# Performance work log

Measured on AMD Instinct MI355X. Metric: run time of the kernel, lower is better.

## Reference

```python
import jax, jax.numpy as jnp
import numpy as np

N_NODES = 100_000
N_EDGES = 3_200_000
IN_FEAT = 512
HIDDEN = 16
N_CLASSES = 7


def setup_inputs() -> dict:
    key = jax.random.key(0)
    kx, ke, kw1, kw2 = jax.random.split(key, 4)
    x = jax.random.normal(kx, (N_NODES, IN_FEAT), dtype=jnp.float32)
    edge_index = jax.random.randint(ke, (2, N_EDGES), 0, N_NODES, dtype=jnp.int64)
    W1 = jax.random.normal(kw1, (IN_FEAT, HIDDEN), dtype=jnp.float32) * (1.0 / np.sqrt(IN_FEAT))
    b1 = jnp.zeros((HIDDEN,), dtype=jnp.float32)
    W2 = jax.random.normal(kw2, (HIDDEN, N_CLASSES), dtype=jnp.float32) * (1.0 / np.sqrt(HIDDEN))
    b2 = jnp.zeros((N_CLASSES,), dtype=jnp.float32)
    return {"x": x, "edge_index": edge_index, "W1": W1, "b1": b1, "W2": W2, "b2": b2}


def _gcn_conv(x, edge_index, W, b):
    """GCNConv: h = D^{-1/2} (A + I) D^{-1/2} (x W) + b  (symmetric normalization, self-loops)."""
    n = x.shape[0]
    h = x @ W  # transform first (small out dim), then aggregate
    loop = jnp.arange(n, dtype=edge_index.dtype)
    src = jnp.concatenate([edge_index[0], loop])  # message sources (incl. self-loops)
    dst = jnp.concatenate([edge_index[1], loop])  # message destinations
    deg = jax.ops.segment_sum(jnp.ones_like(dst, dtype=h.dtype), dst, num_segments=n)
    dinv = jnp.where(deg > 0, jax.lax.rsqrt(deg), 0.0).astype(h.dtype)
    norm = dinv[src] * dinv[dst]                 # [E+N]
    msg = h[src] * norm[:, None]                 # gather + scale
    out = jax.ops.segment_sum(msg, dst, num_segments=n)  # scatter-add
    return out + b


def reference(x, edge_index, W1, b1, W2, b2):
    h = jax.nn.relu(_gcn_conv(x, edge_index, W1, b1))
    # dropout is identity in eval mode
    logits = _gcn_conv(h, edge_index, W2, b2)
    return jax.nn.log_softmax(logits, axis=1)
```

## Files before the change

kernel.cpp:

```cpp
#include <hip/hip_runtime.h>
#include <math.h>

#define TPB 256
#define SCANT 1024

namespace {

constexpr int IN_FEAT = 512;
constexpr int HID = 16;
constexpr int BSH = 8;
constexpr int BSZ = 256;

__device__ inline float4 shfl_xor4(float4 v, int m) {
  v.x = __shfl_xor(v.x, m);
  v.y = __shfl_xor(v.y, m);
  v.z = __shfl_xor(v.z, m);
  v.w = __shfl_xor(v.w, m);
  return v;
}

__global__ void k_detect(const int* __restrict__ ei32, int* __restrict__ flag) {
  __shared__ int red[TPB];
  int t = threadIdx.x;
  int v = 0;
  for (int i = t; i < 2048; i += TPB) v |= ei32[2 * i + 1];
  red[t] = v;
  __syncthreads();
  for (int s = TPB / 2; s > 0; s >>= 1) {
    if (t < s) red[t] |= red[t + s];
    __syncthreads();
  }
  if (t == 0) *flag = (red[0] == 0) ? 1 : 0;
}

__global__ void k_zero_i(int* __restrict__ p, int n) {
  int i = blockIdx.x * TPB + threadIdx.x;
  if (i < n) p[i] = 0;
}

__global__ __launch_bounds__(TPB) void k_binA(const int* __restrict__ ei32,
                                              const long long* __restrict__ ei64,
                                              const int* __restrict__ flag,
                                              int* __restrict__ bucketCnt, int E, int NB) {
  __shared__ int hist[1024];
  int t = threadIdx.x;
  for (int i = t; i < 1024; i += TPB) hist[i] = 0;
  __syncthreads();
  long long e0 = (long long)blockIdx.x * 8192;
  int use64 = *flag;
  for (int j = 0; j < 32; j++) {
    long long e = e0 + j * TPB + t;
    if (e < E) {
      int d = use64 ? (int)ei64[E + e] : ei32[E + e];
      atomicAdd(&hist[d >> BSH], 1);
    }
  }
  __syncthreads();
  for (int b = t; b < NB; b += TPB) {
    int c = hist[b];
    if (c) atomicAdd(&bucketCnt[b], c);
  }
}

__global__ __launch_bounds__(SCANT) void k_binB(const int* __restrict__ bucketCnt,
                                                int* __restrict__ bucketBase,
                                                int* __restrict__ cursor,
                                                int* __restrict__ offsets, int n, int NB) {
  __shared__ int sb[SCANT];
  int t = threadIdx.x;
  int v = (t < NB) ? bucketCnt[t] : 0;
  sb[t] = v;
  __syncthreads();
  for (int off = 1; off < SCANT; off <<= 1) {
    int u = (t >= off) ? sb[t - off] : 0;
    __syncthreads();
    sb[t] += u;
    __syncthreads();
  }
  if (t < NB) {
    int base = sb[t] - v;
    bucketBase[t] = base;
    cursor[t] = base;
  }
  if (t == NB - 1) {
    bucketBase[NB] = sb[t];
    offsets[n] = sb[t];
  }
}

__global__ __launch_bounds__(TPB) void k_binC(const int* __restrict__ ei32,
                                              const long long* __restrict__ ei64,
                                              const int* __restrict__ flag,
                                              int* __restrict__ cursor,
                                              unsigned int* __restrict__ binned, int E, int NB) {
  __shared__ int cnt[1024];
  __shared__ int gbase[1024];
  int t = threadIdx.x;
  for (int i = t; i < 1024; i += TPB) cnt[i] = 0;
  __syncthreads();
  long long e0 = (long long)blockIdx.x * 8192;
  int use64 = *flag;
  for (int j = 0; j < 32; j++) {
    long long e = e0 + j * TPB + t;
    if (e < E) {
      int d = use64 ? (int)ei64[E + e] : ei32[E + e];
      atomicAdd(&cnt[d >> BSH], 1);
    }
  }
  __syncthreads();
  for (int b = t; b < NB; b += TPB) {
    int c = cnt[b];
    gbase[b] = c ? atomicAdd(&cursor[b], c) : 0;
  }
  __syncthreads();
  for (int i = t; i < 1024; i += TPB) cnt[i] = 0;
  __syncthreads();
  for (int j = 0; j < 32; j++) {
    long long e = e0 + j * TPB + t;
    if (e < E) {
      int s, d;
      if (use64) {
        s = (int)ei64[e];
        d = (int)ei64[E + e];
      } else {
        s = ei32[e];
        d = ei32[(long long)E + e];
      }
      int b = d >> BSH;
      int r = atomicAdd(&cnt[b], 1);
      binned[gbase[b] + r] = ((unsigned)(d & (BSZ - 1)) << 24) | (unsigned)s;
    }
  }
}

__global__ __launch_bounds__(TPB) void k_binD(const int* __restrict__ bucketBase,
                                              const unsigned int* __restrict__ binned,
                                              int* __restrict__ offsets, float* __restrict__ dinv,
                                              int* __restrict__ csr, int n) {
  __shared__ int ncnt[256];
  __shared__ int nsc[256];
  __shared__ int ncur[256];
  int t = threadIdx.x;
  int b = blockIdx.x;
  int base = bucketBase[b];
  int cnt = bucketBase[b + 1] - base;
  ncnt[t] = 0;
  __syncthreads();
  for (int i = t; i < cnt; i += TPB) {
    unsigned p = binned[base + i];
    atomicAdd(&ncnt[p >> 24], 1);
  }
  __syncthreads();
  int c = ncnt[t];
  nsc[t] = c;
  __syncthreads();
  for (int off = 1; off < 256; off <<= 1) {
    int u = (t >= off) ? nsc[t - off] : 0;
    __syncthreads();
    nsc[t] += u;
    __syncthreads();
  }
  int excl = nsc[t] - c;
  int node = (b << BSH) + t;
  if (node < n) {
    offsets[node] = base + excl;
    dinv[node] = rsqrtf((float)(c + 1));
  }
  ncur[t] = base + excl;
  __syncthreads();
  for (int i = t; i < cnt; i += TPB) {
    unsigned p = binned[base + i];
    int loc = (int)(p >> 24);
    int pos = atomicAdd(&ncur[loc], 1);
    csr[pos] = (int)(p & 0xFFFFFF);
  }
}

__global__ __launch_bounds__(TPB) void k_gemm1b(const float* __restrict__ x,
                                                const float* __restrict__ W1,
                                                const float* __restrict__ dinv,
                                                float* __restrict__ hs1, int n) {
  __shared__ float xs[192 * 64];
  __shared__ float wt[16 * 68];
  int t = threadIdx.x;
  int rq = t >> 2;
  int cq = t & 3;
  int R0 = blockIdx.x * 192;
  float acc[3][4];
#pragma unroll
  for (int i = 0; i < 3; i++)
#pragma unroll
    for (int c = 0; c < 4; c++) acc[i][c] = 0.f;

  const float4* x4 = (const float4*)x;
  for (int tile = 0; tile < 8; tile++) {
    int k04 = tile << 4;
#pragma unroll
    for (int p = 0; p < 12; p++) {
      int i = p * TPB + t;
      int rr = i >> 4, kk = i & 15;
      int row = R0 + rr;
      if (row > n - 1) row = n - 1;
      float4 v = x4[(long long)row * 128 + k04 + kk];
      *(float4*)&xs[((rr << 4) + (kk ^ (rr & 15))) << 2] = v;
    }
#pragma unroll
    for (int p = 0; p < 4; p++) {
      int i = p * TPB + t;
      int c = i & 15, kf = i >> 4;
      wt[c * 68 + kf] = W1[(((tile << 6) + kf) << 4) + c];
    }
    __syncthreads();
#pragma unroll 4
    for (int kk = 0; kk < 16; kk++) {
      float4 wv[4];
#pragma unroll
      for (int c = 0; c < 4; c++)
        wv[c] = *(const float4*)&wt[(cq * 4 + c) * 68 + (kk << 2)];
#pragma unroll
      for (int i = 0; i < 3; i++) {
        int rr = rq + (i << 6);
        float4 xv = *(const float4*)&xs[((rr << 4) + (kk ^ (rr & 15))) << 2];
#pragma unroll
        for (int c = 0; c < 4; c++) {
          acc[i][c] = fmaf(xv.x, wv[c].x, acc[i][c]);
          acc[i][c] = fmaf(xv.y, wv[c].y, acc[i][c]);
          acc[i][c] = fmaf(xv.z, wv[c].z, acc[i][c]);
          acc[i][c] = fmaf(xv.w, wv[c].w, acc[i][c]);
        }
      }
    }
    __syncthreads();
  }
#pragma unroll
  for (int i = 0; i < 3; i++) {
    int row = R0 + rq + (i << 6);
    if (row < n) {
      float di = dinv[row];
      float4 o = make_float4(acc[i][0] * di, acc[i][1] * di, acc[i][2] * di,
                             acc[i][3] * di);
      *(float4*)&hs1[(long long)row * HID + (cq << 2)] = o;
    }
  }
}

__global__ __launch_bounds__(TPB) void k_agg1f(const int* __restrict__ offsets,
                                               const int* __restrict__ csr,
                                               const float* __restrict__ hs1,
                                               const float* __restrict__ dinv,
                                               const float* __restrict__ b1,
                                               const float* __restrict__ W2,
                                               float* __restrict__ hs2, int n) {
  __shared__ float sW2[112];
  __shared__ float sb1[16];
  int t = threadIdx.x;
  if (t < 112) sW2[t] = W2[t];
  if (t < 16) sb1[t] = b1[t];
  __syncthreads();
  int wid = (int)(((unsigned)blockIdx.x * TPB + t) >> 6);
  if (wid >= n) return;
  int lane = t & 63;
  int q = lane & 3;
  int eg = lane >> 2;
  int s0 = offsets[wid], s1 = offsets[wid + 1];
  float4 acc = make_float4(0.f, 0.f, 0.f, 0.f);
  int e = s0 + eg;
  for (; e + 16 < s1; e += 32) {
    int sA = csr[e], sB = csr[e + 16];
    float4 vA = *(const float4*)(hs1 + ((long long)sA << 4) + (q << 2));
    float4 vB = *(const float4*)(hs1 + ((long long)sB << 4) + (q << 2));
    acc.x += vA.x + vB.x; acc.y += vA.y + vB.y;
    acc.z += vA.z + vB.z; acc.w += vA.w + vB.w;
  }
  if (e < s1) {
    int sA = csr[e];
    float4 vA = *(const float4*)(hs1 + ((long long)sA << 4) + (q << 2));
    acc.x += vA.x; acc.y += vA.y; acc.z += vA.z; acc.w += vA.w;
  }
  for (int m = 4; m < 64; m <<= 1) {
    float4 o = shfl_xor4(acc, m);
    acc.x += o.x; acc.y += o.y; acc.z += o.z; acc.w += o.w;
  }
  float4 sv = *(const float4*)(hs1 + ((long long)wid << 4) + (q << 2));
  float di = dinv[wid];
  int f0 = q << 2;
  float h0 = fmaxf(fmaf(di, acc.x + sv.x, sb1[f0 + 0]), 0.f);
  float h1 = fmaxf(fmaf(di, acc.y + sv.y, sb1[f0 + 1]), 0.f);
  float h2 = fmaxf(fmaf(di, acc.z + sv.z, sb1[f0 + 2]), 0.f);
  float h3 = fmaxf(fmaf(di, acc.w + sv.w, sb1[f0 + 3]), 0.f);
  float o[7];
#pragma unroll
  for (int j = 0; j < 7; j++) {
    float s2 = h0 * sW2[(f0 + 0) * 7 + j];
    s2 = fmaf(h1, sW2[(f0 + 1) * 7 + j], s2);
    s2 = fmaf(h2, sW2[(f0 + 2) * 7 + j], s2);
    s2 = fmaf(h3, sW2[(f0 + 3) * 7 + j], s2);
    o[j] = s2;
  }
#pragma unroll
  for (int m = 1; m < 4; m <<= 1)
#pragma unroll
    for (int j = 0; j < 7; j++) o[j] += __shfl_xor(o[j], m);
  if (lane == 0) {
    float4* hp = (float4*)(hs2 + ((long long)wid << 3));
    hp[0] = make_float4(o[0] * di, o[1] * di, o[2] * di, o[3] * di);
    hp[1] = make_float4(o[4] * di, o[5] * di, o[6] * di, 0.f);
  }
}

__global__ void k_agg2(const int* __restrict__ offsets, const int* __restrict__ csr,
                       const float* __restrict__ hs2, const float* __restrict__ dinv,
                       const float* __restrict__ b2, float* __restrict__ out, int n) {
  int wid = (int)(((unsigned)blockIdx.x * TPB + threadIdx.x) >> 6);
  if (wid >= n) return;
  int lane = threadIdx.x & 63;
  int q = lane & 1;
  int eg = lane >> 1;
  int s0 = offsets[wid], s1 = offsets[wid + 1];
  float4 acc = make_float4(0.f, 0.f, 0.f, 0.f);
  int e = s0 + eg;
  for (; e + 32 < s1; e += 64) {
    int sA = csr[e], sB = csr[e + 32];
    float4 vA = *(const float4*)(hs2 + ((long long)sA << 3) + (q << 2));
    float4 vB = *(const float4*)(hs2 + ((long long)sB << 3) + (q << 2));
    acc.x += vA.x + vB.x; acc.y += vA.y + vB.y;
    acc.z += vA.z + vB.z; acc.w += vA.w + vB.w;
  }
  if (e < s1) {
    int sA = csr[e];
    float4 vA = *(const float4*)(hs2 + ((long long)sA << 3) + (q << 2));
    acc.x += vA.x; acc.y += vA.y; acc.z += vA.z; acc.w += vA.w;
  }
  for (int m = 2; m < 64; m <<= 1) {
    float4 o = shfl_xor4(acc, m);
    acc.x += o.x; acc.y += o.y; acc.z += o.z; acc.w += o.w;
  }
  float4 sv = *(const float4*)(hs2 + ((long long)wid << 3) + (q << 2));
  acc.x += sv.x; acc.y += sv.y; acc.z += sv.z; acc.w += sv.w;
  float di = dinv[wid];
  int f0 = q << 2;
  float vx = fmaf(di, acc.x, b2[f0 + 0]);
  float vy = fmaf(di, acc.y, b2[f0 + 1]);
  float vz = fmaf(di, acc.z, b2[f0 + 2]);
  float vw = (q == 0) ? fmaf(di, acc.w, b2[3]) : 0.f;
  float vw_eff = (q == 0) ? vw : -1e30f;
  float mloc = fmaxf(fmaxf(vx, vy), fmaxf(vz, vw_eff));
  float mm = fmaxf(mloc, __shfl_xor(mloc, 1));
  float sl = expf(vx - mm) + expf(vy - mm) + expf(vz - mm) +
             ((q == 0) ? expf(vw - mm) : 0.f);
  float ss = sl + __shfl_xor(sl, 1);
  float lse = mm + logf(ss);
  if (lane < 2) {
    long long base = (long long)wid * 7 + (q << 2);
    out[base + 0] = vx - lse;
    out[base + 1] = vy - lse;
    out[base + 2] = vz - lse;
    if (q == 0) out[base + 3] = vw - lse;
  }
}

__global__ __launch_bounds__(TPB) void k_gemm1(const float* __restrict__ x,
                                               const float* __restrict__ W1,
                                               const float* __restrict__ dinv,
                                               float* __restrict__ hs1,
                                               float* __restrict__ t1, int n) {
  __shared__ float Wt[HID * IN_FEAT];
  __shared__ float xsl[16 * IN_FEAT];
  int t = threadIdx.x;
  for (int i = t; i < IN_FEAT * HID; i += TPB) {
    int k = i >> 4, c = i & 15;
    int pk = (k >> 2) ^ (c & 7);
    Wt[c * IN_FEAT + (pk << 2) + (k & 3)] = W1[i];
  }
  int c = t >> 4, r = t & 15;
  int xsw = r & 7, wsw = c & 7;
  int ntiles = (n + 15) >> 4;
  for (int tile = blockIdx.x; tile < ntiles; tile += gridDim.x) {
    int r0 = tile << 4;
    for (int i = t; i < 16 * (IN_FEAT / 4); i += TPB) {
      int rr = i >> 7, kk = i & 127;
      int row = r0 + rr;
      if (row > n - 1) row = n - 1;
      float4 v = ((const float4*)x)[(long long)row * (IN_FEAT / 4) + kk];
      *(float4*)&xsl[rr * IN_FEAT + ((kk ^ (rr & 7)) << 2)] = v;
    }
    __syncthreads();
    float acc = 0.f;
#pragma unroll 8
    for (int kk = 0; kk < IN_FEAT / 4; kk++) {
      float4 xv = *(const float4*)&xsl[r * IN_FEAT + ((kk ^ xsw) << 2)];
      float4 wv = *(const float4*)&Wt[c * IN_FEAT + ((kk ^ wsw) << 2)];
      acc = fmaf(xv.x, wv.x, acc);
      acc = fmaf(xv.y, wv.y, acc);
      acc = fmaf(xv.z, wv.z, acc);
      acc = fmaf(xv.w, wv.w, acc);
    }
    int row = r0 + r;
    if (row < n) {
      float val = acc * dinv[row];
      hs1[(long long)row * HID + c] = val;
      if (t1) t1[(long long)row * HID + c] = val;
    }
    __syncthreads();
  }
}

__global__ void k_deg_init(float* __restrict__ deg, int n) {
  int i = blockIdx.x * TPB + threadIdx.x;
  if (i < n) deg[i] = 1.0f;
}

__global__ void k_deg_accum(const int* __restrict__ ei32, const long long* __restrict__ ei64,
                            const int* __restrict__ flag, float* __restrict__ deg, int E) {
  int e = blockIdx.x * TPB + threadIdx.x;
  if (e >= E) return;
  int d = (*flag) ? (int)ei64[(long long)E + e] : ei32[(long long)E + e];
  atomicAdd(&deg[d], 1.0f);
}

__global__ void k_rsqrt(float* __restrict__ deg, int n) {
  int i = blockIdx.x * TPB + threadIdx.x;
  if (i < n) deg[i] = rsqrtf(deg[i]);
}

__global__ void k_scatter1(const int* __restrict__ ei32, const long long* __restrict__ ei64,
                           const int* __restrict__ flag, const float* __restrict__ hs1,
                           float* __restrict__ t1, int E) {
  long long gid = (long long)blockIdx.x * TPB + threadIdx.x;
  long long e = gid >> 4;
  if (e >= E) return;
  int f = (int)(gid & 15);
  int s, d;
  if (*flag) {
    s = (int)ei64[e];
    d = (int)ei64[E + e];
  } else {
    s = ei32[e];
    d = ei32[(long long)E + e];
  }
  atomicAdd(&t1[(long long)d * HID + f], hs1[(long long)s * HID + f]);
}

__global__ void k_layer2(const float* __restrict__ t1, const float* __restrict__ dinv,
                         const float* __restrict__ b1, const float* __restrict__ W2,
                         float* __restrict__ hs2, float* __restrict__ t2, int n) {
  int i = blockIdx.x * TPB + threadIdx.x;
  if (i >= n) return;
  float di = dinv[i];
  float h[16];
  const float4* tp = (const float4*)(t1 + (long long)i * 16);
#pragma unroll
  for (int q = 0; q < 4; q++) {
    float4 v = tp[q];
    float4 b = ((const float4*)b1)[q];
    h[4 * q + 0] = fmaxf(fmaf(di, v.x, b.x), 0.f);
    h[4 * q + 1] = fmaxf(fmaf(di, v.y, b.y), 0.f);
    h[4 * q + 2] = fmaxf(fmaf(di, v.z, b.z), 0.f);
    h[4 * q + 3] = fmaxf(fmaf(di, v.w, b.w), 0.f);
  }
  float o[8];
#pragma unroll
  for (int j = 0; j < 7; j++) {
    float s = 0.f;
#pragma unroll
    for (int cc = 0; cc < 16; cc++) s = fmaf(h[cc], W2[cc * 7 + j], s);
    o[j] = s * di;
  }
  o[7] = 0.f;
  float4 lo = make_float4(o[0], o[1], o[2], o[3]);
  float4 hi = make_float4(o[4], o[5], o[6], o[7]);
  float4* hp = (float4*)(hs2 + (long long)i * 8);
  hp[0] = lo; hp[1] = hi;
  if (t2) {
    float4* qp = (float4*)(t2 + (long long)i * 8);
    qp[0] = lo; qp[1] = hi;
  }
}

__global__ void k_scatter2(const int* __restrict__ ei32, const long long* __restrict__ ei64,
                           const int* __restrict__ flag, const float* __restrict__ hs2,
                           float* __restrict__ t2, int E) {
  long long gid = (long long)blockIdx.x * TPB + threadIdx.x;
  long long e = gid >> 3;
  if (e >= E) return;
  int f = (int)(gid & 7);
  if (f == 7) return;
  int s, d;
  if (*flag) {
    s = (int)ei64[e];
    d = (int)ei64[E + e];
  } else {
    s = ei32[e];
    d = ei32[(long long)E + e];
  }
  atomicAdd(&t2[(long long)d * 8 + f], hs2[(long long)s * 8 + f]);
}

__global__ void k_final(const float* __restrict__ t2, const float* __restrict__ dinv,
                        const float* __restrict__ b2, float* __restrict__ out, int n) {
  int i = blockIdx.x * TPB + threadIdx.x;
  if (i >= n) return;
  float di = dinv[i];
  float v[7];
  float m = -1e30f;
#pragma unroll
  for (int j = 0; j < 7; j++) {
    v[j] = fmaf(di, t2[(long long)i * 8 + j], b2[j]);
    m = fmaxf(m, v[j]);
  }
  float s = 0.f;
#pragma unroll
  for (int j = 0; j < 7; j++) s += expf(v[j] - m);
  float lse = m + logf(s);
#pragma unroll
  for (int j = 0; j < 7; j++) out[(long long)i * 7 + j] = v[j] - lse;
}

}

extern "C" void kernel_launch(void* const* d_in, const int* in_sizes, int n_in,
                              void* d_out, int out_size, void* d_ws, size_t ws_size,
                              hipStream_t stream) {
  const float* x = (const float*)d_in[0];
  const int* ei32 = (const int*)d_in[1];
  const long long* ei64 = (const long long*)d_in[1];
  const float* W1 = (const float*)d_in[2];
  const float* b1 = (const float*)d_in[3];
  const float* W2 = (const float*)d_in[4];
  const float* b2 = (const float*)d_in[5];
  float* out = (float*)d_out;

  int n = in_sizes[0] / IN_FEAT;
  int E = in_sizes[1] / 2;

  int nb_n = (n + TPB - 1) / TPB;
  int nb_e = (E + TPB - 1) / TPB;
  int nb_w = (n + 3) / 4;
  int nb_g = (n + 191) / 192;
  int NB = (n + BSZ - 1) >> BSH;
  int NCH = (int)(((long long)E + 8191) / 8192);

  float* ws = (float*)d_ws;
  int* flag = (int*)d_ws;
  auto align16 = [](long long v) { return (v + 15) & ~15LL; };

  long long w = 64;
  float* dinv = ws + w; w = align16(w + n);
  int* offsets = (int*)(ws + w); w = align16(w + n + 1);
  int* bucketCnt = (int*)(ws + w); w = align16(w + NB);
  int* bucketBase = (int*)(ws + w); w = align16(w + NB + 1);
  int* cursor = (int*)(ws + w); w = align16(w + NB);
  unsigned int* binned = (unsigned int*)(ws + w); w = align16(w + E);
  int* csr = (int*)(ws + w); w = align16(w + E);
  float* hs1 = ws + w; w = align16(w + (long long)n * HID);
  float* hs2 = ws + w; w = align16(w + (long long)n * 8);
  bool bin_ok = (NB >= 1) && (NB <= 1024) && (n <= (1 << 24)) &&
                (ws_size >= (size_t)w * 4);

  if (bin_ok) {
    int nb_nb = (NB + TPB - 1) / TPB;
    hipLaunchKernelGGL(k_detect, dim3(1), dim3(TPB), 0, stream, ei32, flag);
    hipLaunchKernelGGL(k_zero_i, dim3(nb_nb), dim3(TPB), 0, stream, bucketCnt, NB);
    hipLaunchKernelGGL(k_binA, dim3(NCH), dim3(TPB), 0, stream, ei32, ei64, flag, bucketCnt, E,
                       NB);
    hipLaunchKernelGGL(k_binB, dim3(1), dim3(SCANT), 0, stream, bucketCnt, bucketBase, cursor,
                       offsets, n, NB);
    hipLaunchKernelGGL(k_binC, dim3(NCH), dim3(TPB), 0, stream, ei32, ei64, flag, cursor, binned,
                       E, NB);
    hipLaunchKernelGGL(k_binD, dim3(NB), dim3(TPB), 0, stream, bucketBase, binned, offsets, dinv,
                       csr, n);
    hipLaunchKernelGGL(k_gemm1b, dim3(nb_g), dim3(TPB), 0, stream, x, W1, dinv, hs1, n);
    hipLaunchKernelGGL(k_agg1f, dim3(nb_w), dim3(TPB), 0, stream, offsets, csr, hs1, dinv, b1,
                       W2, hs2, n);
    hipLaunchKernelGGL(k_agg2, dim3(nb_w), dim3(TPB), 0, stream, offsets, csr, hs2, dinv, b2,
                       out, n);
  } else {
    float* dinv_f = ws + 64;
    float* hs1_f = dinv_f + n;
    float* t1_f = hs1_f + (long long)n * HID;
    float* hs2_f = t1_f + (long long)n * HID;
    float* t2_f = hs2_f + (long long)n * 8;
    long long w1s = (long long)E * 16, w2s = (long long)E * 8;
    int nb_s1 = (int)((w1s + TPB - 1) / TPB);
    int nb_s2 = (int)((w2s + TPB - 1) / TPB);
    hipLaunchKernelGGL(k_detect, dim3(1), dim3(TPB), 0, stream, ei32, flag);
    hipLaunchKernelGGL(k_deg_init, dim3(nb_n), dim3(TPB), 0, stream, dinv_f, n);
    hipLaunchKernelGGL(k_deg_accum, dim3(nb_e), dim3(TPB), 0, stream, ei32, ei64, flag, dinv_f,
                       E);
    hipLaunchKernelGGL(k_rsqrt, dim3(nb_n), dim3(TPB), 0, stream, dinv_f, n);
    hipLaunchKernelGGL(k_gemm1, dim3(1024), dim3(TPB), 0, stream, x, W1, dinv_f, hs1_f, t1_f, n);
    hipLaunchKernelGGL(k_scatter1, dim3(nb_s1), dim3(TPB), 0, stream, ei32, ei64, flag, hs1_f,
                       t1_f, E);
    hipLaunchKernelGGL(k_layer2, dim3(nb_n), dim3(TPB), 0, stream, t1_f, dinv_f, b1, W2, hs2_f,
                       t2_f, n);
    hipLaunchKernelGGL(k_scatter2, dim3(nb_s2), dim3(TPB), 0, stream, ei32, ei64, flag, hs2_f,
                       t2_f, E);
    hipLaunchKernelGGL(k_final, dim3(nb_n), dim3(TPB), 0, stream, t2_f, dinv_f, b2, out, n);
  }
}
```

Measured before the change: 528.4 us.

## Replace atomic bucket cursors with per-block histogram scan for deterministic binning

The edge-binning pipeline stops using global atomic cursors and a recount pass in the scatter kernel. The first pass now writes a per-block histogram, a column-wise scan over blocks builds per-block offsets, and the scatter kernel reads its bases directly. Bucket size is halved to 128 nodes, which doubles the number of buckets and shrinks the per-bucket CSR build. The chunk size is also reduced so more blocks run the binning passes. In exchange it adds an extra scan kernel and a NCH×NB histogram buffer in the workspace.

```diff
diff --git a/kernel.cpp b/kernel.cpp
--- a/kernel.cpp
+++ b/kernel.cpp
@@ -8,8 +8,8 @@
 
 constexpr int IN_FEAT = 512;
 constexpr int HID = 16;
-constexpr int BSH = 8;
-constexpr int BSZ = 256;
+constexpr int BSH = 7;
+constexpr int BSZ = 128;
 
 __device__ inline float4 shfl_xor4(float4 v, int m) {
   v.x = __shfl_xor(v.x, m);
@@ -33,39 +33,50 @@
   if (t == 0) *flag = (red[0] == 0) ? 1 : 0;
 }
 
-__global__ void k_zero_i(int* __restrict__ p, int n) {
-  int i = blockIdx.x * TPB + threadIdx.x;
-  if (i < n) p[i] = 0;
-}
-
-__global__ __launch_bounds__(TPB) void k_binA(const int* __restrict__ ei32,
-                                              const long long* __restrict__ ei64,
-                                              const int* __restrict__ flag,
-                                              int* __restrict__ bucketCnt, int E, int NB) {
+__global__ __launch_bounds__(TPB) void k_binA2(const int* __restrict__ ei32,
+                                               const long long* __restrict__ ei64,
+                                               const int* __restrict__ flag,
+                                               int* __restrict__ blockHist,
+                                               int E, int NB, int niter) {
   __shared__ int hist[1024];
   int t = threadIdx.x;
   for (int i = t; i < 1024; i += TPB) hist[i] = 0;
   __syncthreads();
-  long long e0 = (long long)blockIdx.x * 8192;
+  long long e0 = (long long)blockIdx.x * niter * TPB;
   int use64 = *flag;
-  for (int j = 0; j < 32; j++) {
-    long long e = e0 + j * TPB + t;
+  for (int j = 0; j < niter; j++) {
+    long long e = e0 + (long long)j * TPB + t;
     if (e < E) {
       int d = use64 ? (int)ei64[E + e] : ei32[E + e];
       atomicAdd(&hist[d >> BSH], 1);
     }
   }
   __syncthreads();
-  for (int b = t; b < NB; b += TPB) {
-    int c = hist[b];
-    if (c) atomicAdd(&bucketCnt[b], c);
-  }
-}
-
-__global__ __launch_bounds__(SCANT) void k_binB(const int* __restrict__ bucketCnt,
-                                                int* __restrict__ bucketBase,
-                                                int* __restrict__ cursor,
-                                                int* __restrict__ offsets, int n, int NB) {
+  long long rb = (long long)blockIdx.x * NB;
+  for (int b = t; b < NB; b += TPB) blockHist[rb + b] = hist[b];
+}
+
+__global__ __launch_bounds__(SCANT) void k_binB1(int* __restrict__ blockHist,
+                                                 int* __restrict__ bucketCnt,
+                                                 int NB, int NCH) {
+  __shared__ int sb[SCANT];
+  int t = threadIdx.x, b = blockIdx.x;
+  int v = (t < NCH) ? blockHist[(long long)t * NB + b] : 0;
+  sb[t] = v;
+  __syncthreads();
+  for (int off = 1; off < SCANT; off <<= 1) {
+    int u = (t >= off) ? sb[t - off] : 0;
+    __syncthreads();
+    sb[t] += u;
+    __syncthreads();
+  }
+  if (t < NCH) blockHist[(long long)t * NB + b] = sb[t] - v;
+  if (t == NCH - 1) bucketCnt[b] = sb[t];
+}
+
+__global__ __launch_bounds__(SCANT) void k_binB2(const int* __restrict__ bucketCnt,
+                                                 int* __restrict__ bucketBase,
+                                                 int* __restrict__ offsets, int n, int NB) {
   __shared__ int sb[SCANT];
   int t = threadIdx.x;
   int v = (t < NB) ? bucketCnt[t] : 0;
@@ -77,46 +88,33 @@
     sb[t] += u;
     __syncthreads();
   }
-  if (t < NB) {
-    int base = sb[t] - v;
-    bucketBase[t] = base;
-    cursor[t] = base;
-  }
+  if (t < NB) bucketBase[t] = sb[t] - v;
   if (t == NB - 1) {
     bucketBase[NB] = sb[t];
     offsets[n] = sb[t];
   }
 }
 
-__global__ __launch_bounds__(TPB) void k_binC(const int* __restrict__ ei32,
-                                              const long long* __restrict__ ei64,
-                                              const int* __restrict__ flag,
-                                              int* __restrict__ cursor,
-                                              unsigned int* __restrict__ binned, int E, int NB) {
-  __shared__ int cnt[1024];
+__global__ __launch_bounds__(TPB) void k_binC2(const int* __restrict__ ei32,
+                                               const long long* __restrict__ ei64,
+                                               const int* __restrict__ flag,
+                                               const int* __restrict__ blockHist,
+                                               const int* __restrict__ bucketBase,
+                                               unsigned int* __restrict__ binned,
+                                               int E, int NB, int niter) {
   __shared__ int gbase[1024];
-  int t = threadIdx.x;
-  for (int i = t; i < 1024; i += TPB) cnt[i] = 0;
-  __syncthreads();
-  long long e0 = (long long)blockIdx.x * 8192;
+  __shared__ int rk[1024];
+  int t = threadIdx.x;
+  long long rb = (long long)blockIdx.x * NB;
+  for (int b = t; b < NB; b += TPB) {
+    gbase[b] = bucketBase[b] + blockHist[rb + b];
+    rk[b] = 0;
+  }
+  __syncthreads();
+  long long e0 = (long long)blockIdx.x * niter * TPB;
   int use64 = *flag;
-  for (int j = 0; j < 32; j++) {
-    long long e = e0 + j * TPB + t;
-    if (e < E) {
-      int d = use64 ? (int)ei64[E + e] : ei32[E + e];
-      atomicAdd(&cnt[d >> BSH], 1);
-    }
-  }
-  __syncthreads();
-  for (int b = t; b < NB; b += TPB) {
-    int c = cnt[b];
-    gbase[b] = c ? atomicAdd(&cursor[b], c) : 0;
-  }
-  __syncthreads();
-  for (int i = t; i < 1024; i += TPB) cnt[i] = 0;
-  __syncthreads();
-  for (int j = 0; j < 32; j++) {
-    long long e = e0 + j * TPB + t;
+  for (int j = 0; j < niter; j++) {
+    long long e = e0 + (long long)j * TPB + t;
     if (e < E) {
       int s, d;
       if (use64) {
@@ -127,8 +125,8 @@
         d = ei32[(long long)E + e];
       }
       int b = d >> BSH;
-      int r = atomicAdd(&cnt[b], 1);
-      binned[gbase[b] + r] = ((unsigned)(d & (BSZ - 1)) << 24) | (unsigned)s;
+      int r = atomicAdd(&rk[b], 1);
+      binned[gbase[b] + r] = ((unsigned)(d & (BSZ - 1)) << 25) | (unsigned)s;
     }
   }
 }
@@ -137,42 +135,43 @@
                                               const unsigned int* __restrict__ binned,
                                               int* __restrict__ offsets, float* __restrict__ dinv,
                                               int* __restrict__ csr, int n) {
-  __shared__ int ncnt[256];
-  __shared__ int nsc[256];
-  __shared__ int ncur[256];
+  __shared__ int ncnt[BSZ];
+  __shared__ int nsc[BSZ];
+  __shared__ int ncur[BSZ];
   int t = threadIdx.x;
   int b = blockIdx.x;
   int base = bucketBase[b];
   int cnt = bucketBase[b + 1] - base;
-  ncnt[t] = 0;
+  if (t < BSZ) ncnt[t] = 0;
+  __syncthreads();
+  for (int i = t; i < cnt; i += TPB) atomicAdd(&ncnt[binned[base + i] >> 25], 1);
+  __syncthreads();
+  int c = 0;
+  if (t < BSZ) {
+    c = ncnt[t];
+    nsc[t] = c;
+  }
+  __syncthreads();
+  for (int off = 1; off < BSZ; off <<= 1) {
+    int u = (t >= off && t < BSZ) ? nsc[t - off] : 0;
+    __syncthreads();
+    if (t < BSZ) nsc[t] += u;
+    __syncthreads();
+  }
+  if (t < BSZ) {
+    int excl = nsc[t] - c;
+    int node = (b << BSH) + t;
+    if (node < n) {
+      offsets[node] = base + excl;
+      dinv[node] = rsqrtf((float)(c + 1));
+    }
+    ncur[t] = base + excl;
+  }
   __syncthreads();
   for (int i = t; i < cnt; i += TPB) {
     unsigned p = binned[base + i];
-    atomicAdd(&ncnt[p >> 24], 1);
-  }
-  __syncthreads();
-  int c = ncnt[t];
-  nsc[t] = c;
-  __syncthreads();
-  for (int off = 1; off < 256; off <<= 1) {
-    int u = (t >= off) ? nsc[t - off] : 0;
-    __syncthreads();
-    nsc[t] += u;
-    __syncthreads();
-  }
-  int excl = nsc[t] - c;
-  int node = (b << BSH) + t;
-  if (node < n) {
-    offsets[node] = base + excl;
-    dinv[node] = rsqrtf((float)(c + 1));
-  }
-  ncur[t] = base + excl;
-  __syncthreads();
-  for (int i = t; i < cnt; i += TPB) {
-    unsigned p = binned[base + i];
-    int loc = (int)(p >> 24);
-    int pos = atomicAdd(&ncur[loc], 1);
-    csr[pos] = (int)(p & 0xFFFFFF);
+    int pos = atomicAdd(&ncur[p >> 25], 1);
+    csr[pos] = (int)(p & 0x1FFFFFF);
   }
 }
 
@@ -538,7 +537,15 @@
   int nb_w = (n + 3) / 4;
   int nb_g = (n + 191) / 192;
   int NB = (n + BSZ - 1) >> BSH;
-  int NCH = (int)(((long long)E + 8191) / 8192);
+
+  int NITER = 16;
+  long long CHUNK = (long long)NITER * TPB;
+  int NCH = (int)((E + CHUNK - 1) / CHUNK);
+  while (NCH > SCANT) {
+    NITER <<= 1;
+    CHUNK = (long long)NITER * TPB;
+    NCH = (int)((E + CHUNK - 1) / CHUNK);
+  }
 
   float* ws = (float*)d_ws;
   int* flag = (int*)d_ws;
@@ -549,24 +556,23 @@
   int* offsets = (int*)(ws + w); w = align16(w + n + 1);
   int* bucketCnt = (int*)(ws + w); w = align16(w + NB);
   int* bucketBase = (int*)(ws + w); w = align16(w + NB + 1);
-  int* cursor = (int*)(ws + w); w = align16(w + NB);
+  int* blockHist = (int*)(ws + w); w = align16(w + (long long)NCH * NB);
   unsigned int* binned = (unsigned int*)(ws + w); w = align16(w + E);
   int* csr = (int*)(ws + w); w = align16(w + E);
   float* hs1 = ws + w; w = align16(w + (long long)n * HID);
   float* hs2 = ws + w; w = align16(w + (long long)n * 8);
-  bool bin_ok = (NB >= 1) && (NB <= 1024) && (n <= (1 << 24)) &&
+  bool bin_ok = (NB >= 1) && (NB <= 1024) && (NCH <= SCANT) && (n <= (1 << 24)) &&
                 (ws_size >= (size_t)w * 4);
 
   if (bin_ok) {
-    int nb_nb = (NB + TPB - 1) / TPB;
     hipLaunchKernelGGL(k_detect, dim3(1), dim3(TPB), 0, stream, ei32, flag);
-    hipLaunchKernelGGL(k_zero_i, dim3(nb_nb), dim3(TPB), 0, stream, bucketCnt, NB);
-    hipLaunchKernelGGL(k_binA, dim3(NCH), dim3(TPB), 0, stream, ei32, ei64, flag, bucketCnt, E,
-                       NB);
-    hipLaunchKernelGGL(k_binB, dim3(1), dim3(SCANT), 0, stream, bucketCnt, bucketBase, cursor,
-                       offsets, n, NB);
-    hipLaunchKernelGGL(k_binC, dim3(NCH), dim3(TPB), 0, stream, ei32, ei64, flag, cursor, binned,
-                       E, NB);
+    hipLaunchKernelGGL(k_binA2, dim3(NCH), dim3(TPB), 0, stream, ei32, ei64, flag, blockHist, E,
+                       NB, NITER);
+    hipLaunchKernelGGL(k_binB1, dim3(NB), dim3(SCANT), 0, stream, blockHist, bucketCnt, NB, NCH);
+    hipLaunchKernelGGL(k_binB2, dim3(1), dim3(SCANT), 0, stream, bucketCnt, bucketBase, offsets,
+                       n, NB);
+    hipLaunchKernelGGL(k_binC2, dim3(NCH), dim3(TPB), 0, stream, ei32, ei64, flag, blockHist,
+                       bucketBase, binned, E, NB, NITER);
     hipLaunchKernelGGL(k_binD, dim3(NB), dim3(TPB), 0, stream, bucketBase, binned, offsets, dinv,
                        csr, n);
     hipLaunchKernelGGL(k_gemm1b, dim3(nb_g), dim3(TPB), 0, stream, x, W1, dinv, hs1, n);
```

Result: no change. 528.7 us (+0.1%).
